# Performance work log

Measured on AMD Instinct MI355X. Metric: run time of the kernel, lower is better.

Reference implementation:

```python
import jax, jax.numpy as jnp
import numpy as np

COMMITMENT_COST = 0.25
NUM_EMBEDDINGS = 1024
EMB_DIMS = [64, 128, 256]
RES = [(96, 320), (48, 160), (24, 80)]
BATCH = 8


def setup_inputs() -> dict:
    key = jax.random.key(0)
    ks = jax.random.split(key, 6)
    inp = {}
    for i, (d, (h, w)) in enumerate(zip(EMB_DIMS, RES)):
        inp[f"x{i}"] = jax.random.normal(ks[i], (BATCH, d, h, w), dtype=jnp.float32)
        inp[f"emb{i}"] = jax.random.normal(ks[3 + i], (NUM_EMBEDDINGS, d), dtype=jnp.float32)
    return inp


def _quantize_level(x, emb):
    # x: [B, D, H, W], emb: [K, D]
    B, D, H, W = x.shape
    xf = jnp.transpose(x, (0, 2, 3, 1)).reshape(-1, D)  # [N, D]
    dist = (
        jnp.sum(xf * xf, axis=1, keepdims=True)
        + jnp.sum(emb * emb, axis=1)
        - 2.0 * xf @ emb.T
    )
    idx = jnp.argmin(dist, axis=1)  # [N]
    q = emb[idx]  # gather == one-hot @ emb in the original
    # commitment loss (quantized is detached in e_latent_loss)
    loss = COMMITMENT_COST * jnp.mean((jax.lax.stop_gradient(q) - xf) ** 2)
    # straight-through estimator
    q_st = xf + jax.lax.stop_gradient(q - xf)
    q_out = jnp.transpose(q_st.reshape(B, H, W, D), (0, 3, 1, 2))  # back to NCHW
    return loss, q_out


def reference(x0, x1, x2, emb0, emb1, emb2):
    # eval-mode MultiCodebook.forward (return_indices=False, return_features=False)
    total_loss = jnp.float32(0.0)
    feats = []
    for x, emb in ((x0, emb0), (x1, emb1), (x2, emb2)):
        loss, q = _quantize_level(x, emb)
        total_loss = total_loss + loss
        feats.append(q)
    return (total_loss, feats[0], feats[1], feats[2])
```

## Files before the change

kernel.cpp:

```cpp
#include <hip/hip_runtime.h>
#include <float.h>

typedef __bf16 bf16x8 __attribute__((ext_vector_type(8)));
typedef float  f32x16 __attribute__((ext_vector_type(16)));

#define WS_EE    0
#define WS_SLOT  12288
#define WS_IMG0  16384
#define WS_IMG1  (WS_IMG0 + 4096 * 64)
#define WS_IMG2  (WS_IMG1 + 4096 * 128)

__device__ __forceinline__ short f2bf(float f) {
    unsigned u = __float_as_uint(f);
    unsigned r = (u + 0x7FFFu + ((u >> 16) & 1u)) >> 16;
    return (short)r;
}
__device__ __forceinline__ float bf2f(short s) {
    return __uint_as_float(((unsigned)(unsigned short)s) << 16);
}
__device__ __forceinline__ unsigned pk2(short a, short b) {
    return (unsigned)(unsigned short)a | ((unsigned)(unsigned short)b << 16);
}

__global__ void ee_all(const float* __restrict__ e0, const float* __restrict__ e1,
                       const float* __restrict__ e2, float* __restrict__ ee)
{
    int bid = blockIdx.x;
    const float* e; float* o; int D;
    if (bid < 256)      { e = e0; o = ee;        D = 64;  }
    else if (bid < 512) { e = e1; o = ee + 1024; D = 128; bid -= 256; }
    else                { e = e2; o = ee + 2048; D = 256; bid -= 512; }
    int k  = bid * 4 + (threadIdx.x >> 6);
    int ln = threadIdx.x & 63;
    float s = 0.f;
    for (int d = ln; d < D; d += 64) { float v = e[(size_t)k * D + d]; s = fmaf(v, v, s); }
#pragma unroll
    for (int m = 32; m >= 1; m >>= 1) s += __shfl_xor(s, m);
    if (ln == 0) o[k] = s;
}

__global__ void prep_emb(const float* __restrict__ e0, const float* __restrict__ e1,
                         const float* __restrict__ e2, char* __restrict__ ws)
{
    int flat = blockIdx.x * 256 + threadIdx.x;
    const float* emb; char* img; int D, id;
    if (flat < 8192)       { emb = e0; img = ws + WS_IMG0; D = 64;  id = flat; }
    else if (flat < 24576) { emb = e1; img = ws + WS_IMG1; D = 128; id = flat - 8192; }
    else                   { emb = e2; img = ws + WS_IMG2; D = 256; id = flat - 24576; }
    int chunks = D >> 3;
    int c  = id / chunks;
    int ch = id - c * chunks;
    int d0 = ch * 8;
    int kc = d0 >> 6;
    int dd = d0 & 63;
    int q  = ((dd >> 4) << 2) + (((dd >> 3) & 1) << 1);
    int r  = c & 127;
    int ct = c >> 7;
    const float* s = emb + (size_t)c * D + d0;
    unsigned hw[4], lw[4];
#pragma unroll
    for (int j = 0; j < 4; ++j) {
        float va = s[2 * j], vb = s[2 * j + 1];
        short ha = f2bf(va), hb = f2bf(vb);
        short la = f2bf(va - bf2f(ha)), lb = f2bf(vb - bf2f(hb));
        hw[j] = pk2(ha, hb);
        lw[j] = pk2(la, lb);
    }
    char* base = img + ((size_t)(ct * (D >> 6) + kc)) * 32768 + r * 256;
    *(uint4*)(base + ((q       ^ (r & 7)) << 4)) = make_uint4(hw[0], hw[1], hw[2], hw[3]);
    *(uint4*)(base + (((q + 1) ^ (r & 7)) << 4)) = make_uint4(lw[0], lw[1], lw[2], lw[3]);
}

__shared__ __align__(16) short g_x[16384];
__shared__ __align__(16) short g_e[16384];
__shared__ float g_m1[128];
__shared__ float g_m2[128];
__shared__ int   g_i1[128];
__shared__ int   g_sidx[128];
__shared__ float g_d1[128];
__shared__ int   g_flag[130];
__shared__ unsigned long long g_red;
__shared__ float g_part[4];

template<int D, int HW, int PTS>
__device__ void vq_core2(const float* __restrict__ x, const float* __restrict__ emb,
                         const float* __restrict__ eesq, const char* __restrict__ eimg,
                         float* __restrict__ feat, float* __restrict__ slots,
                         float lscale, float margin, int ptblk)
{
    constexpr int KCS  = D / 64;
    constexpr int ROWG = PTS / 32;
    constexpr int TPW  = ROWG;
    constexpr int W    = 4 / ROWG;

    const int tid  = threadIdx.x;
    const int L    = tid & 63;
    const int wave = tid >> 6;
    const int col  = L & 31;
    const int half = L >> 5;
    const int rowg = wave % ROWG;
    const int cgrp = wave / ROWG;

    const int pt0 = ptblk * PTS;
    const int b   = pt0 / HW;
    const int hw0 = pt0 % HW;
    const float* xb = x + (size_t)b * D * HW + hw0;

    float ssq = 0.f;
#pragma unroll
    for (int it = 0; it < 4; ++it) {
        int flat = it * 256 + tid;
        int pt   = flat % PTS;
        int dch  = flat / PTS;
        int d0   = dch * 8;
        int kc   = d0 >> 6;
        int dd   = d0 & 63;
        int q    = ((dd >> 4) << 2) + (((dd >> 3) & 1) << 1);
        unsigned hw_[4], lw_[4];
#pragma unroll
        for (int j = 0; j < 4; ++j) {
            float va = xb[(size_t)(d0 + 2 * j)     * HW + pt];
            float vb = xb[(size_t)(d0 + 2 * j + 1) * HW + pt];
            ssq = fmaf(va, va, ssq);
            ssq = fmaf(vb, vb, ssq);
            short ha = f2bf(va), hb = f2bf(vb);
            short la = f2bf(va - bf2f(ha)), lb = f2bf(vb - bf2f(hb));
            hw_[j] = pk2(ha, hb);
            lw_[j] = pk2(la, lb);
        }
        short* row = g_x + kc * (PTS * 128) + pt * 128;
        *(uint4*)(row + (((q    ) ^ (pt & 7)) << 3)) = make_uint4(hw_[0], hw_[1], hw_[2], hw_[3]);
        *(uint4*)(row + (((q + 1) ^ (pt & 7)) << 3)) = make_uint4(lw_[0], lw_[1], lw_[2], lw_[3]);
    }
    if (tid == 0) g_flag[0] = 0;

    float m1[16], m2[16]; int i1[16];
#pragma unroll
    for (int r = 0; r < 16; ++r) { m1[r] = FLT_MAX; m2[r] = FLT_MAX; i1[r] = 0; }

    const int arow = rowg * 32 + col;
    const short* xrow0 = g_x + arow * 128;

    for (int cg = 0; cg < 8; ++cg) {
        f32x16 acc[TPW];
#pragma unroll
        for (int t = 0; t < TPW; ++t)
#pragma unroll
            for (int j = 0; j < 16; ++j) acc[t][j] = 0.f;

        for (int kc = 0; kc < KCS; ++kc) {
            __syncthreads();
            const uint4* esrc = (const uint4*)(eimg + (size_t)(cg * KCS + kc) * 32768);
            uint4* edst = (uint4*)g_e;
#pragma unroll
            for (int it = 0; it < 8; ++it) {
                int g = it * 256 + tid;
                edst[g] = esrc[g];
            }
            __syncthreads();

            const short* xck = xrow0 + kc * (PTS * 128);
#pragma unroll
            for (int t4 = 0; t4 < 4; ++t4) {
                int qh = t4 * 4 + half * 2;
                bf16x8 ah = *(const bf16x8*)(xck + (((qh    ) ^ (arow & 7)) << 3));
                bf16x8 al = *(const bf16x8*)(xck + (((qh + 1) ^ (arow & 7)) << 3));
#pragma unroll
                for (int t = 0; t < TPW; ++t) {
                    int brow = (cgrp * TPW + t) * 32 + col;
                    const short* br = g_e + brow * 128;
                    bf16x8 bh = *(const bf16x8*)(br + (((qh    ) ^ (brow & 7)) << 3));
                    bf16x8 bl = *(const bf16x8*)(br + (((qh + 1) ^ (brow & 7)) << 3));
                    acc[t] = __builtin_amdgcn_mfma_f32_32x32x16_bf16(ah, bh, acc[t], 0, 0, 0);
                    acc[t] = __builtin_amdgcn_mfma_f32_32x32x16_bf16(ah, bl, acc[t], 0, 0, 0);
                    acc[t] = __builtin_amdgcn_mfma_f32_32x32x16_bf16(al, bh, acc[t], 0, 0, 0);
                }
            }
        }

#pragma unroll
        for (int t = 0; t < TPW; ++t) {
            int c = cg * 128 + (cgrp * TPW + t) * 32 + col;
            float eec = eesq[c];
#pragma unroll
            for (int r = 0; r < 16; ++r) {
                float dist = fmaf(-2.f, acc[t][r], eec);
                m2[r] = __builtin_amdgcn_fmed3f(dist, m1[r], m2[r]);
                bool lt = dist < m1[r];
                m1[r] = lt ? dist : m1[r];
                i1[r] = lt ? c : i1[r];
            }
        }
    }

#pragma unroll
    for (int r = 0; r < 16; ++r) {
#pragma unroll
        for (int msk = 1; msk <= 16; msk <<= 1) {
            float om1 = __shfl_xor(m1[r], msk);
            int   oi  = __shfl_xor(i1[r], msk);
            float om2 = __shfl_xor(m2[r], msk);
            float mx  = fmaxf(m1[r], om1);
            m2[r] = fminf(mx, fminf(m2[r], om2));
            bool tk = (om1 < m1[r]) || (om1 == m1[r] && oi < i1[r]);
            m1[r] = tk ? om1 : m1[r];
            i1[r] = tk ? oi  : i1[r];
        }
    }
#pragma unroll
    for (int r = 0; r < 16; ++r) {
        int r16 = (r & 3) + 8 * (r >> 2) + 4 * half;
        if (col == r16) {
            int p = rowg * 32 + r16;
            g_m1[p * W + cgrp] = m1[r];
            g_m2[p * W + cgrp] = m2[r];
            g_i1[p * W + cgrp] = i1[r];
        }
    }
    __syncthreads();

    if (tid < PTS) {
        float bm1 = FLT_MAX, bm2 = FLT_MAX; int bi = 0x7FFFFFFF;
#pragma unroll
        for (int s = 0; s < W; ++s) {
            float am1 = g_m1[tid * W + s];
            float am2 = g_m2[tid * W + s];
            int   ai  = g_i1[tid * W + s];
            float mx  = fmaxf(bm1, am1);
            bm2 = fminf(mx, fminf(bm2, am2));
            bool tk = (am1 < bm1) || (am1 == bm1 && ai < bi);
            bm1 = tk ? am1 : bm1;
            bi  = tk ? ai  : bi;
        }
        g_sidx[tid] = bi;
        g_d1[tid]   = bm1;
        if (bm2 - bm1 <= margin) {
            int pos = atomicAdd(&g_flag[0], 1);
            g_flag[1 + pos] = tid;
        }
    }
    __syncthreads();

    int nf = g_flag[0];
    float* sx = (float*)g_e;
    for (int i = 0; i < nf; ++i) {
        int p   = g_flag[1 + i];
        int phw = hw0 + p;
        for (int d = tid; d < D; d += 256) sx[d] = x[((size_t)b * D + d) * HW + phw];
        if (tid == 0) g_red = ~0ull;
        __syncthreads();
#pragma unroll
        for (int j = 0; j < 4; ++j) {
            int c = j * 256 + tid;
            float s = 0.f;
#pragma unroll 4
            for (int d = 0; d < D; ++d) s = fmaf(sx[d], emb[(size_t)c * D + d], s);
            float dist = fmaf(-2.f, s, eesq[c]);
            unsigned u = __float_as_uint(dist);
            u = (u >> 31) ? ~u : (u | 0x80000000u);
            unsigned long long pkv = ((unsigned long long)u << 32) | (unsigned)c;
            atomicMin(&g_red, pkv);
        }
        __syncthreads();
        if (tid == 0) {
            unsigned u = (unsigned)(g_red >> 32);
            unsigned orig = (u & 0x80000000u) ? (u ^ 0x80000000u) : ~u;
            g_sidx[p] = (int)(g_red & 0xFFFFFFFFu);
            g_d1[p]   = __uint_as_float(orig);
        }
        __syncthreads();
    }

#pragma unroll 4
    for (int it = 0; it < (PTS * D) / 256; ++it) {
        int flat = it * 256 + tid;
        int p  = flat % PTS;
        int dd = flat / PTS;
        int k  = g_sidx[p];
        feat[((size_t)b * D + dd) * HW + hw0 + p] = emb[(size_t)k * D + dd];
    }

    float lsum = ssq;
    if (tid < PTS) lsum += g_d1[tid];
#pragma unroll
    for (int m = 32; m >= 1; m >>= 1) lsum += __shfl_xor(lsum, m);
    if (L == 0) g_part[wave] = lsum;
    __syncthreads();
    if (tid == 0) {
        float tot = (g_part[0] + g_part[1]) + (g_part[2] + g_part[3]);
        atomicAdd(&slots[blockIdx.x & 127], tot * lscale);
    }
}

__global__ __launch_bounds__(256, 2)
void vq_main2(const float* __restrict__ x0, const float* __restrict__ e0,
              const float* __restrict__ x1, const float* __restrict__ e1,
              const float* __restrict__ x2, const float* __restrict__ e2,
              char* __restrict__ ws,
              float* __restrict__ f0, float* __restrict__ f1, float* __restrict__ f2)
{
    const float* ee = (const float*)ws;
    float* slots = (float*)(ws + WS_SLOT);
    int bid = blockIdx.x;
    if (bid < 480) {
        vq_core2<256, 1920, 32>(x2, e2, ee + 2048, ws + WS_IMG2, f2, slots,
                                0.25f / 3932160.f, 8e-3f, bid);
    } else if (bid < 1440) {
        vq_core2<128, 7680, 64>(x1, e1, ee + 1024, ws + WS_IMG1, f1, slots,
                                0.25f / 7864320.f, 5e-3f, bid - 480);
    } else {
        vq_core2<64, 30720, 128>(x0, e0, ee, ws + WS_IMG0, f0, slots,
                                 0.25f / 15728640.f, 4e-3f, bid - 1440);
    }
}

__global__ void loss_finish(const float* __restrict__ slots, float* __restrict__ out)
{
    int t = threadIdx.x;
    float v = slots[t];
#pragma unroll
    for (int m = 32; m >= 1; m >>= 1) v += __shfl_xor(v, m);
    __shared__ float p2[2];
    if ((t & 63) == 0) p2[t >> 6] = v;
    __syncthreads();
    if (t == 0) out[0] = p2[0] + p2[1];
}

extern "C" void kernel_launch(void* const* d_in, const int* in_sizes, int n_in,
                              void* d_out, int out_size, void* d_ws, size_t ws_size,
                              hipStream_t stream)
{
    const float* x0 = (const float*)d_in[0];
    const float* e0 = (const float*)d_in[1];
    const float* x1 = (const float*)d_in[2];
    const float* e1 = (const float*)d_in[3];
    const float* x2 = (const float*)d_in[4];
    const float* e2 = (const float*)d_in[5];

    float* out  = (float*)d_out;
    float* f0   = out + 1;
    float* f1   = f0 + 15728640;
    float* f2   = f1 + 7864320;

    char* ws = (char*)d_ws;
    float* eef   = (float*)ws;
    float* slots = (float*)(ws + WS_SLOT);

    hipMemsetAsync(slots, 0, 128 * sizeof(float), stream);

    ee_all<<<768, 256, 0, stream>>>(e0, e1, e2, eef);
    prep_emb<<<224, 256, 0, stream>>>(e0, e1, e2, ws);

    vq_main2<<<3360, 256, 0, stream>>>(x0, e0, x1, e1, x2, e2, ws, f0, f1, f2);

    loss_finish<<<1, 128, 0, stream>>>(slots, out);
}
```

Measured before the change: 528.4 us.

## Double-buffer codebook tiles with async global-to-LDS loads and register-resident x fragments

```diff
diff --git a/kernel.cpp b/kernel.cpp
--- a/kernel.cpp
+++ b/kernel.cpp
@@ -22,27 +22,40 @@
     return (unsigned)(unsigned short)a | ((unsigned)(unsigned short)b << 16);
 }
 
-__global__ void ee_all(const float* __restrict__ e0, const float* __restrict__ e1,
-                       const float* __restrict__ e2, float* __restrict__ ee)
+__device__ __forceinline__ void stage_tile(const char* __restrict__ src, short* dst, int tid)
+{
+    const char* s = src + tid * 16;
+    char* d = (char*)dst + tid * 16;
+#pragma unroll
+    for (int it = 0; it < 8; ++it) {
+        __builtin_amdgcn_global_load_lds(
+            (const __attribute__((address_space(1))) void*)(s + it * 4096),
+            (__attribute__((address_space(3))) void*)(d + it * 4096),
+            16, 0, 0);
+    }
+}
+
+__global__ void prep_all(const float* __restrict__ e0, const float* __restrict__ e1,
+                         const float* __restrict__ e2, char* __restrict__ ws)
 {
     int bid = blockIdx.x;
-    const float* e; float* o; int D;
-    if (bid < 256)      { e = e0; o = ee;        D = 64;  }
-    else if (bid < 512) { e = e1; o = ee + 1024; D = 128; bid -= 256; }
-    else                { e = e2; o = ee + 2048; D = 256; bid -= 512; }
-    int k  = bid * 4 + (threadIdx.x >> 6);
-    int ln = threadIdx.x & 63;
-    float s = 0.f;
-    for (int d = ln; d < D; d += 64) { float v = e[(size_t)k * D + d]; s = fmaf(v, v, s); }
-#pragma unroll
-    for (int m = 32; m >= 1; m >>= 1) s += __shfl_xor(s, m);
-    if (ln == 0) o[k] = s;
-}
-
-__global__ void prep_emb(const float* __restrict__ e0, const float* __restrict__ e1,
-                         const float* __restrict__ e2, char* __restrict__ ws)
-{
-    int flat = blockIdx.x * 256 + threadIdx.x;
+    if (bid >= 224) {
+        int b2 = bid - 224;
+        float* ee = (float*)ws;
+        const float* e; float* o; int D;
+        if (b2 < 256)      { e = e0; o = ee;        D = 64;  }
+        else if (b2 < 512) { e = e1; o = ee + 1024; D = 128; b2 -= 256; }
+        else               { e = e2; o = ee + 2048; D = 256; b2 -= 512; }
+        int k  = b2 * 4 + (threadIdx.x >> 6);
+        int ln = threadIdx.x & 63;
+        float s = 0.f;
+        for (int d = ln; d < D; d += 64) { float v = e[(size_t)k * D + d]; s = fmaf(v, v, s); }
+#pragma unroll
+        for (int m = 32; m >= 1; m >>= 1) s += __shfl_xor(s, m);
+        if (ln == 0) o[k] = s;
+        return;
+    }
+    int flat = bid * 256 + threadIdx.x;
     const float* emb; char* img; int D, id;
     if (flat < 8192)       { emb = e0; img = ws + WS_IMG0; D = 64;  id = flat; }
     else if (flat < 24576) { emb = e1; img = ws + WS_IMG1; D = 128; id = flat - 8192; }
@@ -67,12 +80,13 @@
         lw[j] = pk2(la, lb);
     }
     char* base = img + ((size_t)(ct * (D >> 6) + kc)) * 32768 + r * 256;
-    *(uint4*)(base + ((q       ^ (r & 7)) << 4)) = make_uint4(hw[0], hw[1], hw[2], hw[3]);
-    *(uint4*)(base + (((q + 1) ^ (r & 7)) << 4)) = make_uint4(lw[0], lw[1], lw[2], lw[3]);
-}
-
-__shared__ __align__(16) short g_x[16384];
-__shared__ __align__(16) short g_e[16384];
+    *(uint4*)(base + (((q    ) ^ (r & 15)) << 4)) = make_uint4(hw[0], hw[1], hw[2], hw[3]);
+    *(uint4*)(base + (((q + 1) ^ (r & 15)) << 4)) = make_uint4(lw[0], lw[1], lw[2], lw[3]);
+}
+
+__shared__ __align__(16) short g_eb0[16384];
+__shared__ __align__(16) short g_eb1[16384];
+__shared__ __align__(16) float g_ee[1024];
 __shared__ float g_m1[128];
 __shared__ float g_m2[128];
 __shared__ int   g_i1[128];
@@ -83,7 +97,7 @@
 __shared__ float g_part[4];
 
 template<int D, int HW, int PTS>
-__device__ void vq_core2(const float* __restrict__ x, const float* __restrict__ emb,
+__device__ void vq_core3(const float* __restrict__ x, const float* __restrict__ emb,
                          const float* __restrict__ eesq, const char* __restrict__ eimg,
                          float* __restrict__ feat, float* __restrict__ slots,
                          float lscale, float margin, int ptblk)
@@ -92,6 +106,8 @@
     constexpr int ROWG = PTS / 32;
     constexpr int TPW  = ROWG;
     constexpr int W    = 4 / ROWG;
+    constexpr int NT   = 8 * KCS;
+    constexpr bool SA  = (TPW <= 2);
 
     const int tid  = threadIdx.x;
     const int L    = tid & 63;
@@ -106,6 +122,9 @@
     const int hw0 = pt0 % HW;
     const float* xb = x + (size_t)b * D * HW + hw0;
 
+    stage_tile(eimg, g_eb1, tid);
+
+    short* gx = g_eb0;
     float ssq = 0.f;
 #pragma unroll
     for (int it = 0; it < 4; ++it) {
@@ -128,63 +147,102 @@
             hw_[j] = pk2(ha, hb);
             lw_[j] = pk2(la, lb);
         }
-        short* row = g_x + kc * (PTS * 128) + pt * 128;
-        *(uint4*)(row + (((q    ) ^ (pt & 7)) << 3)) = make_uint4(hw_[0], hw_[1], hw_[2], hw_[3]);
-        *(uint4*)(row + (((q + 1) ^ (pt & 7)) << 3)) = make_uint4(lw_[0], lw_[1], lw_[2], lw_[3]);
-    }
+        short* row = gx + kc * (PTS * 128) + pt * 128;
+        *(uint4*)(row + (((q    ) ^ (pt & 15)) << 3)) = make_uint4(hw_[0], hw_[1], hw_[2], hw_[3]);
+        *(uint4*)(row + (((q + 1) ^ (pt & 15)) << 3)) = make_uint4(lw_[0], lw_[1], lw_[2], lw_[3]);
+    }
+#pragma unroll
+    for (int i = 0; i < 4; ++i) g_ee[i * 256 + tid] = eesq[i * 256 + tid];
     if (tid == 0) g_flag[0] = 0;
 
+    asm volatile("s_waitcnt lgkmcnt(0)" ::: "memory");
+    __builtin_amdgcn_s_barrier();
+    __builtin_amdgcn_sched_barrier(0);
+
+    const int arow = rowg * 32 + col;
+    const short* xrow0 = gx + arow * 128;
+    bf16x8 afh[KCS][4], afl[KCS][4];
+#pragma unroll
+    for (int kc = 0; kc < KCS; ++kc) {
+        const short* xck = xrow0 + kc * (PTS * 128);
+#pragma unroll
+        for (int t4 = 0; t4 < 4; ++t4) {
+            int qh = t4 * 4 + half * 2;
+            afh[kc][t4] = *(const bf16x8*)(xck + (((qh    ) ^ (arow & 15)) << 3));
+            afl[kc][t4] = *(const bf16x8*)(xck + (((qh + 1) ^ (arow & 15)) << 3));
+        }
+    }
+    asm volatile("s_waitcnt lgkmcnt(0)" ::: "memory");
+    __builtin_amdgcn_s_barrier();
+    __builtin_amdgcn_sched_barrier(0);
+    stage_tile(eimg + 32768, g_eb0, tid);
+
     float m1[16], m2[16]; int i1[16];
 #pragma unroll
     for (int r = 0; r < 16; ++r) { m1[r] = FLT_MAX; m2[r] = FLT_MAX; i1[r] = 0; }
 
-    const int arow = rowg * 32 + col;
-    const short* xrow0 = g_x + arow * 128;
-
     for (int cg = 0; cg < 8; ++cg) {
+        float eecv[TPW];
+#pragma unroll
+        for (int tt = 0; tt < TPW; ++tt)
+            eecv[tt] = g_ee[cg * 128 + (cgrp * TPW + tt) * 32 + col];
+
         f32x16 acc[TPW];
-#pragma unroll
-        for (int t = 0; t < TPW; ++t)
-#pragma unroll
-            for (int j = 0; j < 16; ++j) acc[t][j] = 0.f;
-
+        f32x16 acc2[SA ? TPW : 1];
+#pragma unroll
+        for (int tt = 0; tt < TPW; ++tt)
+#pragma unroll
+            for (int j = 0; j < 16; ++j) acc[tt][j] = 0.f;
+        if constexpr (SA) {
+#pragma unroll
+            for (int tt = 0; tt < TPW; ++tt)
+#pragma unroll
+                for (int j = 0; j < 16; ++j) acc2[tt][j] = 0.f;
+        }
+
+#pragma unroll
         for (int kc = 0; kc < KCS; ++kc) {
-            __syncthreads();
-            const uint4* esrc = (const uint4*)(eimg + (size_t)(cg * KCS + kc) * 32768);
-            uint4* edst = (uint4*)g_e;
-#pragma unroll
-            for (int it = 0; it < 8; ++it) {
-                int g = it * 256 + tid;
-                edst[g] = esrc[g];
-            }
-            __syncthreads();
-
-            const short* xck = xrow0 + kc * (PTS * 128);
+            const int t = cg * KCS + kc;
+            short* buft = (t & 1) ? g_eb0 : g_eb1;
+            if (t == NT - 1) asm volatile("s_waitcnt vmcnt(0)" ::: "memory");
+            else             asm volatile("s_waitcnt vmcnt(8)" ::: "memory");
+            __builtin_amdgcn_s_barrier();
+            __builtin_amdgcn_sched_barrier(0);
 #pragma unroll
             for (int t4 = 0; t4 < 4; ++t4) {
-                int qh = t4 * 4 + half * 2;
-                bf16x8 ah = *(const bf16x8*)(xck + (((qh    ) ^ (arow & 7)) << 3));
-                bf16x8 al = *(const bf16x8*)(xck + (((qh + 1) ^ (arow & 7)) << 3));
-#pragma unroll
-                for (int t = 0; t < TPW; ++t) {
-                    int brow = (cgrp * TPW + t) * 32 + col;
-                    const short* br = g_e + brow * 128;
-                    bf16x8 bh = *(const bf16x8*)(br + (((qh    ) ^ (brow & 7)) << 3));
-                    bf16x8 bl = *(const bf16x8*)(br + (((qh + 1) ^ (brow & 7)) << 3));
-                    acc[t] = __builtin_amdgcn_mfma_f32_32x32x16_bf16(ah, bh, acc[t], 0, 0, 0);
-                    acc[t] = __builtin_amdgcn_mfma_f32_32x32x16_bf16(ah, bl, acc[t], 0, 0, 0);
-                    acc[t] = __builtin_amdgcn_mfma_f32_32x32x16_bf16(al, bh, acc[t], 0, 0, 0);
+                const int qh = t4 * 4 + half * 2;
+#pragma unroll
+                for (int tt = 0; tt < TPW; ++tt) {
+                    const int brow = (cgrp * TPW + tt) * 32 + col;
+                    const short* br = buft + brow * 128;
+                    bf16x8 bh = *(const bf16x8*)(br + (((qh    ) ^ (brow & 15)) << 3));
+                    bf16x8 bl = *(const bf16x8*)(br + (((qh + 1) ^ (brow & 15)) << 3));
+                    if constexpr (SA) {
+                        acc [tt] = __builtin_amdgcn_mfma_f32_32x32x16_bf16(afh[kc][t4], bh, acc [tt], 0, 0, 0);
+                        acc2[tt] = __builtin_amdgcn_mfma_f32_32x32x16_bf16(afh[kc][t4], bl, acc2[tt], 0, 0, 0);
+                        acc2[tt] = __builtin_amdgcn_mfma_f32_32x32x16_bf16(afl[kc][t4], bh, acc2[tt], 0, 0, 0);
+                    } else {
+                        acc[tt] = __builtin_amdgcn_mfma_f32_32x32x16_bf16(afh[kc][t4], bh, acc[tt], 0, 0, 0);
+                        acc[tt] = __builtin_amdgcn_mfma_f32_32x32x16_bf16(afh[kc][t4], bl, acc[tt], 0, 0, 0);
+                        acc[tt] = __builtin_amdgcn_mfma_f32_32x32x16_bf16(afl[kc][t4], bh, acc[tt], 0, 0, 0);
+                    }
                 }
             }
-        }
-
-#pragma unroll
-        for (int t = 0; t < TPW; ++t) {
-            int c = cg * 128 + (cgrp * TPW + t) * 32 + col;
-            float eec = eesq[c];
+            asm volatile("s_waitcnt lgkmcnt(0)" ::: "memory");
+            __builtin_amdgcn_s_barrier();
+            __builtin_amdgcn_sched_barrier(0);
+            if (t + 2 < NT) stage_tile(eimg + (size_t)(t + 2) * 32768, buft, tid);
+        }
+
+#pragma unroll
+        for (int tt = 0; tt < TPW; ++tt) {
+            int c = cg * 128 + (cgrp * TPW + tt) * 32 + col;
+            float eec = eecv[tt];
 #pragma unroll
             for (int r = 0; r < 16; ++r) {
-                float dist = fmaf(-2.f, acc[t][r], eec);
+                float av = acc[tt][r];
+                if constexpr (SA) av += acc2[tt][r];
+                float dist = fmaf(-2.f, av, eec);
                 m2[r] = __builtin_amdgcn_fmed3f(dist, m1[r], m2[r]);
                 bool lt = dist < m1[r];
                 m1[r] = lt ? dist : m1[r];
@@ -242,7 +300,7 @@
     __syncthreads();
 
     int nf = g_flag[0];
-    float* sx = (float*)g_e;
+    float* sx = (float*)g_eb0;
     for (int i = 0; i < nf; ++i) {
         int p   = g_flag[1 + i];
         int phw = hw0 + p;
@@ -255,7 +313,7 @@
             float s = 0.f;
 #pragma unroll 4
             for (int d = 0; d < D; ++d) s = fmaf(sx[d], emb[(size_t)c * D + d], s);
-            float dist = fmaf(-2.f, s, eesq[c]);
+            float dist = fmaf(-2.f, s, g_ee[c]);
             unsigned u = __float_as_uint(dist);
             u = (u >> 31) ? ~u : (u | 0x80000000u);
             unsigned long long pkv = ((unsigned long long)u << 32) | (unsigned)c;
@@ -293,7 +351,7 @@
 }
 
 __global__ __launch_bounds__(256, 2)
-void vq_main2(const float* __restrict__ x0, const float* __restrict__ e0,
+void vq_main3(const float* __restrict__ x0, const float* __restrict__ e0,
               const float* __restrict__ x1, const float* __restrict__ e1,
               const float* __restrict__ x2, const float* __restrict__ e2,
               char* __restrict__ ws,
@@ -303,13 +361,13 @@
     float* slots = (float*)(ws + WS_SLOT);
     int bid = blockIdx.x;
     if (bid < 480) {
-        vq_core2<256, 1920, 32>(x2, e2, ee + 2048, ws + WS_IMG2, f2, slots,
+        vq_core3<256, 1920, 32>(x2, e2, ee + 2048, ws + WS_IMG2, f2, slots,
                                 0.25f / 3932160.f, 8e-3f, bid);
     } else if (bid < 1440) {
-        vq_core2<128, 7680, 64>(x1, e1, ee + 1024, ws + WS_IMG1, f1, slots,
+        vq_core3<128, 7680, 64>(x1, e1, ee + 1024, ws + WS_IMG1, f1, slots,
                                 0.25f / 7864320.f, 5e-3f, bid - 480);
     } else {
-        vq_core2<64, 30720, 128>(x0, e0, ee, ws + WS_IMG0, f0, slots,
+        vq_core3<64, 30720, 128>(x0, e0, ee, ws + WS_IMG0, f0, slots,
                                  0.25f / 15728640.f, 4e-3f, bid - 1440);
     }
 }
@@ -343,15 +401,13 @@
     float* f2   = f1 + 7864320;
 
     char* ws = (char*)d_ws;
-    float* eef   = (float*)ws;
     float* slots = (float*)(ws + WS_SLOT);
 
     hipMemsetAsync(slots, 0, 128 * sizeof(float), stream);
 
-    ee_all<<<768, 256, 0, stream>>>(e0, e1, e2, eef);
-    prep_emb<<<224, 256, 0, stream>>>(e0, e1, e2, ws);
-
-    vq_main2<<<3360, 256, 0, stream>>>(x0, e0, x1, e1, x2, e2, ws, f0, f1, f2);
+    prep_all<<<992, 256, 0, stream>>>(e0, e1, e2, ws);
+
+    vq_main3<<<3360, 256, 0, stream>>>(x0, e0, x1, e1, x2, e2, ws, f0, f1, f2);
 
     loss_finish<<<1, 128, 0, stream>>>(slots, out);
 }
```

Result: no change. 522.0 us (-1.2%).
